# Kernel optimization log

Measured on AMD Instinct MI355X. Metric: run time of the kernel, lower is better.

Reference implementation:

```python
import jax, jax.numpy as jnp
import numpy as np

B, S, I, R, O = 32, 4096, 64, 1024, 8
SPECTRAL_RADIUS = 0.95


def setup_inputs() -> dict:
    key = jax.random.key(0)
    k1, k2, k3, k4 = jax.random.split(key, 4)
    x = jax.random.normal(k1, (B, S, I), dtype=jnp.float32)
    W_in = jax.random.uniform(k2, (R, I), dtype=jnp.float32) - 0.5
    W_res = jax.random.uniform(k3, (R, R), dtype=jnp.float32) - 0.5
    # rescale W_res so its spectral radius equals SPECTRAL_RADIUS (as in __init__)
    radius = SPECTRAL_RADIUS / float(np.max(np.abs(np.linalg.eigvals(np.asarray(W_res)))))
    W_res = W_res * jnp.float32(radius)
    # original inits W_out to zeros; use small random values so output is non-trivial
    W_out = jax.random.normal(k4, (O, R + I), dtype=jnp.float32) * 0.02
    return {"x": x, "W_in": W_in, "W_res": W_res, "W_out": W_out}


def reference(x, W_in, W_res, W_out):
    # Precompute input drive for all timesteps: [B, S, R]
    pre = jnp.einsum('bsi,ri->bsr', x, W_in)

    def step(r, p_t):
        # r: [B, R], p_t: [B, R]
        r = jnp.tanh(p_t + r @ W_res.T)
        return r, r

    r0 = jnp.zeros((x.shape[0], W_res.shape[0]), dtype=x.dtype)
    _, rs = jax.lax.scan(step, r0, jnp.swapaxes(pre, 0, 1))  # rs: [S, B, R]
    rs = jnp.swapaxes(rs, 0, 1)                               # [B, S, R]
    feats = jnp.concatenate([x, rs], axis=-1)                 # [B, S, I+R]
    out = jnp.einsum('bsf,of->bso', feats, W_out)             # [B, S, O]
    return jnp.squeeze(out)
```

## Files before the change

### kernel.cpp

```cpp
#include <hip/hip_runtime.h>
#include <hip/hip_fp16.h>
#include <math.h>


#define NS 4096
#define NI 64
#define NR 1024
#define NO 8
#define NB 32
#define NGRP 8
#define GPP 32
#define CPG 4
#define WROWS 32
#define NT 512
#define XPAD 68
#define RPH (NB * NR / 2)

typedef __fp16 h2 __attribute__((ext_vector_type(2)));
union UH2 { unsigned u; h2 h; };

#define ATSU(p,v) __hip_atomic_store((p), (v), __ATOMIC_RELAXED, __HIP_MEMORY_SCOPE_AGENT)
#define ATLU(p)   __hip_atomic_load((p), __ATOMIC_RELAXED, __HIP_MEMORY_SCOPE_AGENT)
#define ATAU(p,v) __hip_atomic_fetch_add((p), (v), __ATOMIC_RELAXED, __HIP_MEMORY_SCOPE_AGENT)

static __device__ __forceinline__ h2 u2h(unsigned u) { UH2 t; t.u = u; return t.h; }

static __device__ __forceinline__ float fast_tanh(float x) {
  x = fminf(fmaxf(x, -20.f), 20.f);
  float e = __builtin_amdgcn_exp2f(x * 2.8853900817779268f);
  return (e - 1.0f) * __builtin_amdgcn_rcpf(e + 1.0f);
}

__global__ void init_cnt_kernel(unsigned int* cnt) {
  const int t = threadIdx.x;
  cnt[t] = 0u; cnt[t + 1024] = 0u; cnt[t + 2048] = 0u; cnt[t + 3072] = 0u;
}

__global__ __launch_bounds__(NT)
__attribute__((amdgpu_waves_per_eu(2, 2)))
void esn_scan(const float* __restrict__ x, const float* __restrict__ Win,
              const float* __restrict__ Wres, const float* __restrict__ Wout,
              float* __restrict__ out, unsigned int* __restrict__ cnt,
              unsigned int* __restrict__ rbuf_h)
{
  extern __shared__ float dynpad[];
  const int wg  = blockIdx.x;
  const int g   = wg & 7;
  const int m   = wg >> 3;
  const int tid = threadIdx.x;
  const int w   = tid >> 6;
  const int l   = tid & 63;

  __shared__ unsigned r_h[CPG][NR / 2];
  __shared__ float x_lds[3][CPG][XPAD];
  __shared__ float win_s[WROWS][XPAD];
  __shared__ unsigned woutr_h[NO][NR / 2];
  __shared__ float woutx_s[NO][NI];

  if (x[0] == 1234.5678f) { dynpad[tid] = 1.f; out[tid] = dynpad[tid ^ 1]; }

  h2 wh[32];
  {
    const int grow0 = 32 * m + 4 * w;
    #pragma unroll
    for (int r = 0; r < 4; ++r)
      #pragma unroll
      for (int s = 0; s < 4; ++s) {
        float4 t4 = *(const float4*)&Wres[(size_t)(grow0 + r) * NR + 4 * l + 256 * s];
        wh[(r * 4 + s) * 2 + 0] = __builtin_amdgcn_cvt_pkrtz(t4.x, t4.y);
        wh[(r * 4 + s) * 2 + 1] = __builtin_amdgcn_cvt_pkrtz(t4.z, t4.w);
      }
  }
  for (int idx = tid; idx < WROWS * NI; idx += NT) {
    int rr = idx >> 6, ii = idx & 63;
    win_s[rr][ii] = Win[(32 * m + rr) * NI + ii];
  }
  for (int idx = tid; idx < NO * (NR / 2); idx += NT) {
    int o = idx >> 9, p = idx & 511;
    UH2 t; t.h = __builtin_amdgcn_cvt_pkrtz(Wout[o * (NI + NR) + NI + 2 * p],
                                            Wout[o * (NI + NR) + NI + 2 * p + 1]);
    woutr_h[o][p] = t.u;
  }
  if (tid < NO * NI) {
    int o = tid >> 6, ii = tid & 63;
    woutx_s[o][ii] = Wout[o * (NI + NR) + ii];
  }
  if (tid < 256) {
    const int c = tid >> 6, ii = tid & 63;
    x_lds[0][c][ii] = x[(size_t)(4 * g + c) * NS * NI + ii];
  }
  __syncthreads();

  unsigned int* bcp = cnt + (g * 8 + (m & 7)) * 64;

  for (int t = 0; t < NS; ++t) {
    const int par = t & 1, pprev = par ^ 1;

    unsigned uv0, uv1, uv2, uv3;
    if (t > 0) {
      const unsigned* rq = rbuf_h + (size_t)pprev * RPH + (size_t)g * 2048 + 4 * tid;
      uv0 = ATLU(rq);     uv1 = ATLU(rq + 1);
      uv2 = ATLU(rq + 2); uv3 = ATLU(rq + 3);
    } else {
      uv0 = uv1 = uv2 = uv3 = 0u;
    }

    float pin;
    {
      const int p = l & 15;
      const int prow = 4 * w + (p >> 2);
      const int pc = p & 3;
      const int cb = (l >> 4) * 16;
      const float* wr = &win_s[prow][cb];
      const float* xr = &x_lds[t % 3][pc][cb];
      float4 a0 = *(const float4*)&wr[0];
      float4 a1 = *(const float4*)&wr[4];
      float4 a2 = *(const float4*)&wr[8];
      float4 a3 = *(const float4*)&wr[12];
      float4 b0 = *(const float4*)&xr[0];
      float4 b1 = *(const float4*)&xr[4];
      float4 b2 = *(const float4*)&xr[8];
      float4 b3 = *(const float4*)&xr[12];
      pin = a0.x * b0.x;
      pin = fmaf(a0.y, b0.y, pin); pin = fmaf(a0.z, b0.z, pin);
      pin = fmaf(a0.w, b0.w, pin);
      pin = fmaf(a1.x, b1.x, pin); pin = fmaf(a1.y, b1.y, pin);
      pin = fmaf(a1.z, b1.z, pin); pin = fmaf(a1.w, b1.w, pin);
      pin = fmaf(a2.x, b2.x, pin); pin = fmaf(a2.y, b2.y, pin);
      pin = fmaf(a2.z, b2.z, pin); pin = fmaf(a2.w, b2.w, pin);
      pin = fmaf(a3.x, b3.x, pin); pin = fmaf(a3.y, b3.y, pin);
      pin = fmaf(a3.z, b3.z, pin); pin = fmaf(a3.w, b3.w, pin);
      pin += __shfl_xor(pin, 16);
      pin += __shfl_xor(pin, 32);
    }

    r_h[0][tid] = uv0; r_h[1][tid] = uv1;
    r_h[2][tid] = uv2; r_h[3][tid] = uv3;
    __syncthreads();

    float acc[4][4];
    #pragma unroll
    for (int r = 0; r < 4; ++r)
      #pragma unroll
      for (int c = 0; c < 4; ++c) acc[r][c] = 0.f;
    #pragma unroll
    for (int s = 0; s < 4; ++s) {
      uint2 q0 = *(const uint2*)&r_h[0][2 * l + 128 * s];
      uint2 q1 = *(const uint2*)&r_h[1][2 * l + 128 * s];
      uint2 q2 = *(const uint2*)&r_h[2][2 * l + 128 * s];
      uint2 q3 = *(const uint2*)&r_h[3][2 * l + 128 * s];
      #pragma unroll
      for (int r = 0; r < 4; ++r) {
        const h2 wa = wh[(r * 4 + s) * 2 + 0];
        const h2 wb = wh[(r * 4 + s) * 2 + 1];
        acc[r][0] = __builtin_amdgcn_fdot2(wa, u2h(q0.x), acc[r][0], false);
        acc[r][0] = __builtin_amdgcn_fdot2(wb, u2h(q0.y), acc[r][0], false);
        acc[r][1] = __builtin_amdgcn_fdot2(wa, u2h(q1.x), acc[r][1], false);
        acc[r][1] = __builtin_amdgcn_fdot2(wb, u2h(q1.y), acc[r][1], false);
        acc[r][2] = __builtin_amdgcn_fdot2(wa, u2h(q2.x), acc[r][2], false);
        acc[r][2] = __builtin_amdgcn_fdot2(wb, u2h(q2.y), acc[r][2], false);
        acc[r][3] = __builtin_amdgcn_fdot2(wa, u2h(q3.x), acc[r][3], false);
        acc[r][3] = __builtin_amdgcn_fdot2(wb, u2h(q3.y), acc[r][3], false);
      }
    }

    float v[16];
    #pragma unroll
    for (int k = 0; k < 16; ++k) v[k] = acc[k >> 2][k & 3];
    #pragma unroll
    for (int lev = 0; lev < 4; ++lev) {
      const int d = 1 << lev;
      const int n = 16 >> lev;
      #pragma unroll
      for (int i = 0; i < n / 2; ++i) {
        float a  = v[2 * i]     + __shfl_xor(v[2 * i],     d);
        float bb = v[2 * i + 1] + __shfl_xor(v[2 * i + 1], d);
        v[i] = (l & d) ? bb : a;
      }
    }
    float dsum = v[0];
    dsum += __shfl_xor(dsum, 16);
    dsum += __shfl_xor(dsum, 32);

    {
      float rv = fast_tanh(dsum + pin);
      float rvo = __shfl_xor(rv, 4);
      if (l < 16 && ((l >> 2) & 1) == 0) {
        const int r = l >> 2, c = l & 3;
        UH2 hp; hp.h = __builtin_amdgcn_cvt_pkrtz(rv, rvo);
        const int pair = 16 * m + 2 * w + (r >> 1);
        ATSU(rbuf_h + (size_t)par * RPH + (size_t)g * 2048 + 4 * pair + c, hp.u);
      }
    }

    __syncthreads();
    if (tid == 0) ATAU(bcp, 1u);

    if (t + 1 < NS && tid < 256) {
      const int c = tid >> 6, ii = tid & 63;
      x_lds[(t + 1) % 3][c][ii] = x[((size_t)(4 * g + c) * NS + (t + 1)) * NI + ii];
    }
    if (t > 0 && m == ((t - 1) & 31)) {
      const int grp = tid >> 4;
      const int j   = tid & 15;
      const int c   = grp >> 3, o = grp & 7;
      float s = 0.f;
      #pragma unroll
      for (int k = 0; k < 16; ++k) {
        uint2 rr = *(const uint2*)&r_h[c][32 * k + 2 * j];
        uint2 ww = *(const uint2*)&woutr_h[o][32 * k + 2 * j];
        s = __builtin_amdgcn_fdot2(u2h(rr.x), u2h(ww.x), s, false);
        s = __builtin_amdgcn_fdot2(u2h(rr.y), u2h(ww.y), s, false);
      }
      #pragma unroll
      for (int e = 0; e < 4; ++e)
        s = fmaf(woutx_s[o][4 * j + e], x_lds[(t + 2) % 3][c][4 * j + e], s);
      s += __shfl_xor(s, 1); s += __shfl_xor(s, 2);
      s += __shfl_xor(s, 4); s += __shfl_xor(s, 8);
      if (j == 0) out[((size_t)(4 * g + c) * NS + (t - 1)) * NO + o] = s;
    }

    if (w == 0) {
      const unsigned tg = 4u * (unsigned)(t + 1);
      const unsigned* pa = cnt + (g * 8 + (l & 7)) * 64;
      while (!__all((int)(ATLU(pa) >= tg))) { }
    }
    __syncthreads();
  }

  if (m == 31) {
    const int fpar = (NS - 1) & 1;
    const unsigned* rq = rbuf_h + (size_t)fpar * RPH + (size_t)g * 2048 + 4 * tid;
    r_h[0][tid] = ATLU(rq);
    r_h[1][tid] = ATLU(rq + 1);
    r_h[2][tid] = ATLU(rq + 2);
    r_h[3][tid] = ATLU(rq + 3);
    __syncthreads();
    const int grp = tid >> 4;
    const int j   = tid & 15;
    const int c   = grp >> 3, o = grp & 7;
    float s = 0.f;
    #pragma unroll
    for (int k = 0; k < 16; ++k) {
      uint2 rr = *(const uint2*)&r_h[c][32 * k + 2 * j];
      uint2 ww = *(const uint2*)&woutr_h[o][32 * k + 2 * j];
      s = __builtin_amdgcn_fdot2(u2h(rr.x), u2h(ww.x), s, false);
      s = __builtin_amdgcn_fdot2(u2h(rr.y), u2h(ww.y), s, false);
    }
    #pragma unroll
    for (int e = 0; e < 4; ++e)
      s = fmaf(woutx_s[o][4 * j + e], x_lds[(NS - 1) % 3][c][4 * j + e], s);
    s += __shfl_xor(s, 1); s += __shfl_xor(s, 2);
    s += __shfl_xor(s, 4); s += __shfl_xor(s, 8);
    if (j == 0) out[((size_t)(4 * g + c) * NS + (NS - 1)) * NO + o] = s;
  }
}

extern "C" void kernel_launch(void* const* d_in, const int* in_sizes, int n_in,
                              void* d_out, int out_size, void* d_ws, size_t ws_size,
                              hipStream_t stream) {
  const float* x    = (const float*)d_in[0];
  const float* Win  = (const float*)d_in[1];
  const float* Wres = (const float*)d_in[2];
  const float* Wout = (const float*)d_in[3];
  float* out = (float*)d_out;

  char* ws = (char*)d_ws;
  unsigned int* cnt = (unsigned int*)ws;
  unsigned int* rbuf_h = (unsigned int*)(ws + 16384);

  hipLaunchKernelGGL(init_cnt_kernel, dim3(1), dim3(1024), 0, stream, cnt);
  hipLaunchKernelGGL(esn_scan, dim3(256), dim3(NT), 64 * 1024, stream,
                     x, Win, Wres, Wout, out, cnt, rbuf_h);
}
```

Baseline: 11.16 ms.

## Replace counter barrier with timestep-tagged 64-bit data packets for cross-block sync

Each published fp16 pair of reservoir state is now stored as a 64-bit word carrying the timestep in its high half. Consumers spin on the data itself until the tags match. This removes the separate per-group atomic counter increment, the extra __syncthreads before it, and the wave-0 spin on counters. The exchange layout is reorganized per batch column and doubles the memory written per step. Consumers may also poll many words instead of a few counters, which adds memory traffic while waiting.

Result: slower. 12.54 ms (+12.3%).

```diff
diff --git a/kernel.cpp b/kernel.cpp
--- a/kernel.cpp
+++ b/kernel.cpp
@@ -14,14 +14,13 @@
 #define WROWS 32
 #define NT 512
 #define XPAD 68
-#define RPH (NB * NR / 2)
+#define RSLAB 16384
 
 typedef __fp16 h2 __attribute__((ext_vector_type(2)));
 union UH2 { unsigned u; h2 h; };
 
-#define ATSU(p,v) __hip_atomic_store((p), (v), __ATOMIC_RELAXED, __HIP_MEMORY_SCOPE_AGENT)
-#define ATLU(p)   __hip_atomic_load((p), __ATOMIC_RELAXED, __HIP_MEMORY_SCOPE_AGENT)
-#define ATAU(p,v) __hip_atomic_fetch_add((p), (v), __ATOMIC_RELAXED, __HIP_MEMORY_SCOPE_AGENT)
+#define ATSU64(p,v) __hip_atomic_store((p), (v), __ATOMIC_RELAXED, __HIP_MEMORY_SCOPE_AGENT)
+#define ATLU64(p)   __hip_atomic_load((p), __ATOMIC_RELAXED, __HIP_MEMORY_SCOPE_AGENT)
 
 static __device__ __forceinline__ h2 u2h(unsigned u) { UH2 t; t.u = u; return t.h; }
 
@@ -31,17 +30,15 @@
   return (e - 1.0f) * __builtin_amdgcn_rcpf(e + 1.0f);
 }
 
-__global__ void init_cnt_kernel(unsigned int* cnt) {
-  const int t = threadIdx.x;
-  cnt[t] = 0u; cnt[t + 1024] = 0u; cnt[t + 2048] = 0u; cnt[t + 3072] = 0u;
+__global__ void init_rbuf_kernel(unsigned long long* rbuf_e) {
+  rbuf_e[(size_t)blockIdx.x * 1024 + threadIdx.x] = 0ull;
 }
 
 __global__ __launch_bounds__(NT)
 __attribute__((amdgpu_waves_per_eu(2, 2)))
 void esn_scan(const float* __restrict__ x, const float* __restrict__ Win,
               const float* __restrict__ Wres, const float* __restrict__ Wout,
-              float* __restrict__ out, unsigned int* __restrict__ cnt,
-              unsigned int* __restrict__ rbuf_h)
+              float* __restrict__ out, unsigned long long* __restrict__ rbuf_e)
 {
   extern __shared__ float dynpad[];
   const int wg  = blockIdx.x;
@@ -91,18 +88,17 @@
   }
   __syncthreads();
 
-  unsigned int* bcp = cnt + (g * 8 + (m & 7)) * 64;
-
   for (int t = 0; t < NS; ++t) {
     const int par = t & 1, pprev = par ^ 1;
 
-    unsigned uv0, uv1, uv2, uv3;
+    unsigned long long e0 = 0ull, e1 = 0ull, e2 = 0ull, e3 = 0ull;
+    const unsigned long long* rq = rbuf_e + (size_t)pprev * RSLAB
+                                 + (size_t)(4 * g) * 512 + tid;
     if (t > 0) {
-      const unsigned* rq = rbuf_h + (size_t)pprev * RPH + (size_t)g * 2048 + 4 * tid;
-      uv0 = ATLU(rq);     uv1 = ATLU(rq + 1);
-      uv2 = ATLU(rq + 2); uv3 = ATLU(rq + 3);
-    } else {
-      uv0 = uv1 = uv2 = uv3 = 0u;
+      e0 = ATLU64(rq);
+      e1 = ATLU64(rq + 512);
+      e2 = ATLU64(rq + 1024);
+      e3 = ATLU64(rq + 1536);
     }
 
     float pin;
@@ -134,8 +130,23 @@
       pin += __shfl_xor(pin, 32);
     }
 
-    r_h[0][tid] = uv0; r_h[1][tid] = uv1;
-    r_h[2][tid] = uv2; r_h[3][tid] = uv3;
+    if (t > 0) {
+      const unsigned tg = (unsigned)t;
+      for (;;) {
+        const bool s0 = (unsigned)(e0 >> 32) != tg;
+        const bool s1 = (unsigned)(e1 >> 32) != tg;
+        const bool s2 = (unsigned)(e2 >> 32) != tg;
+        const bool s3 = (unsigned)(e3 >> 32) != tg;
+        if (!(s0 | s1 | s2 | s3)) break;
+        if (s0) e0 = ATLU64(rq);
+        if (s1) e1 = ATLU64(rq + 512);
+        if (s2) e2 = ATLU64(rq + 1024);
+        if (s3) e3 = ATLU64(rq + 1536);
+      }
+    }
+
+    r_h[0][tid] = (unsigned)e0; r_h[1][tid] = (unsigned)e1;
+    r_h[2][tid] = (unsigned)e2; r_h[3][tid] = (unsigned)e3;
     __syncthreads();
 
     float acc[4][4];
@@ -185,16 +196,15 @@
     {
       float rv = fast_tanh(dsum + pin);
       float rvo = __shfl_xor(rv, 4);
+      UH2 hp; hp.h = __builtin_amdgcn_cvt_pkrtz(rv, rvo);
       if (l < 16 && ((l >> 2) & 1) == 0) {
         const int r = l >> 2, c = l & 3;
-        UH2 hp; hp.h = __builtin_amdgcn_cvt_pkrtz(rv, rvo);
-        const int pair = 16 * m + 2 * w + (r >> 1);
-        ATSU(rbuf_h + (size_t)par * RPH + (size_t)g * 2048 + 4 * pair + c, hp.u);
-      }
-    }
-
-    __syncthreads();
-    if (tid == 0) ATAU(bcp, 1u);
+        const int word = 16 * m + 2 * w + (r >> 1);
+        const unsigned long long pkt =
+          (((unsigned long long)(unsigned)(t + 1)) << 32) | (unsigned long long)hp.u;
+        ATSU64(rbuf_e + (size_t)par * RSLAB + (size_t)(4 * g + c) * 512 + word, pkt);
+      }
+    }
 
     if (t + 1 < NS && tid < 256) {
       const int c = tid >> 6, ii = tid & 63;
@@ -220,21 +230,29 @@
       if (j == 0) out[((size_t)(4 * g + c) * NS + (t - 1)) * NO + o] = s;
     }
 
-    if (w == 0) {
-      const unsigned tg = 4u * (unsigned)(t + 1);
-      const unsigned* pa = cnt + (g * 8 + (l & 7)) * 64;
-      while (!__all((int)(ATLU(pa) >= tg))) { }
-    }
     __syncthreads();
   }
 
   if (m == 31) {
     const int fpar = (NS - 1) & 1;
-    const unsigned* rq = rbuf_h + (size_t)fpar * RPH + (size_t)g * 2048 + 4 * tid;
-    r_h[0][tid] = ATLU(rq);
-    r_h[1][tid] = ATLU(rq + 1);
-    r_h[2][tid] = ATLU(rq + 2);
-    r_h[3][tid] = ATLU(rq + 3);
+    const unsigned long long* rq = rbuf_e + (size_t)fpar * RSLAB
+                                 + (size_t)(4 * g) * 512 + tid;
+    unsigned long long e0 = ATLU64(rq),        e1 = ATLU64(rq + 512);
+    unsigned long long e2 = ATLU64(rq + 1024), e3 = ATLU64(rq + 1536);
+    const unsigned tg = (unsigned)NS;
+    for (;;) {
+      const bool s0 = (unsigned)(e0 >> 32) != tg;
+      const bool s1 = (unsigned)(e1 >> 32) != tg;
+      const bool s2 = (unsigned)(e2 >> 32) != tg;
+      const bool s3 = (unsigned)(e3 >> 32) != tg;
+      if (!(s0 | s1 | s2 | s3)) break;
+      if (s0) e0 = ATLU64(rq);
+      if (s1) e1 = ATLU64(rq + 512);
+      if (s2) e2 = ATLU64(rq + 1024);
+      if (s3) e3 = ATLU64(rq + 1536);
+    }
+    r_h[0][tid] = (unsigned)e0; r_h[1][tid] = (unsigned)e1;
+    r_h[2][tid] = (unsigned)e2; r_h[3][tid] = (unsigned)e3;
     __syncthreads();
     const int grp = tid >> 4;
     const int j   = tid & 15;
@@ -265,11 +283,9 @@
   const float* Wout = (const float*)d_in[3];
   float* out = (float*)d_out;
 
-  char* ws = (char*)d_ws;
-  unsigned int* cnt = (unsigned int*)ws;
-  unsigned int* rbuf_h = (unsigned int*)(ws + 16384);
-
-  hipLaunchKernelGGL(init_cnt_kernel, dim3(1), dim3(1024), 0, stream, cnt);
+  unsigned long long* rbuf_e = (unsigned long long*)d_ws;
+
+  hipLaunchKernelGGL(init_rbuf_kernel, dim3(32), dim3(1024), 0, stream, rbuf_e);
   hipLaunchKernelGGL(esn_scan, dim3(256), dim3(NT), 64 * 1024, stream,
-                     x, Win, Wres, Wout, out, cnt, rbuf_h);
-}
+                     x, Win, Wres, Wout, out, rbuf_e);
+}
```
